# Kernel tuning notes

Hardware: AMD Instinct MI355X
Metric: run time of the kernel (lower is better)

## Reference

```python
import jax, jax.numpy as jnp
import numpy as np

B, S, E, H = 4, 2048, 1024, 16
D = E // H  # head dim = 64


def setup_inputs() -> dict:
    key = jax.random.key(0)
    ks = jax.random.split(key, 5)
    s = 0.02
    return {
        "x": jax.random.normal(ks[0], (B, S, E), dtype=jnp.float32),
        "Wq": jax.random.normal(ks[1], (E, E), dtype=jnp.float32) * s,
        "Wk": jax.random.normal(ks[2], (E, E), dtype=jnp.float32) * s,
        "Wv": jax.random.normal(ks[3], (E, E), dtype=jnp.float32) * s,
        "Wo": jax.random.normal(ks[4], (E, E), dtype=jnp.float32) * s,
        "bo": jnp.zeros((E,), dtype=jnp.float32),
    }


def reference(x, Wq, Wk, Wv, Wo, bo):
    b, s, e = x.shape
    h, d = H, e // H
    # QKV projections -> [b, h, s, d]
    q = (x @ Wq).reshape(b, s, h, d).transpose(0, 2, 1, 3)
    k = (x @ Wk).reshape(b, s, h, d).transpose(0, 2, 1, 3)
    v = (x @ Wv).reshape(b, s, h, d).transpose(0, 2, 1, 3)
    # scores [b, h, s, s], causal mask with -inf, scaled softmax
    a = jnp.einsum('bhqd,bhkd->bhqk', q, k)
    causal = jnp.tril(jnp.ones((s, s), dtype=bool))  # True where allowed
    a = jnp.where(causal, a, -jnp.inf) / jnp.sqrt(jnp.asarray(d, x.dtype))
    a = jax.nn.softmax(a, axis=-1)
    # dropout p=0.0 (identity in eval)
    y = jnp.einsum('bhqk,bhkd->bhqd', a, v)
    y = y.transpose(0, 2, 1, 3).reshape(b, s, e)
    return y @ Wo + bo
```

## Files before the change

kernel.cpp:

```cpp
#include <hip/hip_runtime.h>

typedef __bf16 bf16x8 __attribute__((ext_vector_type(8)));
typedef float f32x4 __attribute__((ext_vector_type(4)));
typedef unsigned short u16x8 __attribute__((ext_vector_type(8)));

#define S_LEN 2048
#define NHEAD 16
#define HDIM  64
#define EMB   1024

__device__ __forceinline__ ushort f2b(float v) {
  union { float f; unsigned u; } x; x.f = v;
  unsigned r = (x.u + 0x7fffu + ((x.u >> 16) & 1u)) >> 16;
  return (ushort)r;
}

__device__ __forceinline__ ushort f2b_trunc(float v) {
  union { float f; unsigned u; } x; x.f = v;
  return (ushort)(x.u >> 16);
}

typedef const __attribute__((address_space(1))) unsigned int* gp1_t;
typedef __attribute__((address_space(3))) unsigned int* lp3_t;
__device__ __forceinline__ void gld16(const ushort* g, const ushort* l) {
  __builtin_amdgcn_global_load_lds((gp1_t)(unsigned long long)(uintptr_t)g,
                                   (lp3_t)(unsigned int)(uintptr_t)l, 16, 0, 0);
}

__global__ __launch_bounds__(256) void prep_kernel(
    const float* __restrict__ x, const float* __restrict__ W0,
    const float* __restrict__ W1, const float* __restrict__ W2,
    const float* __restrict__ W3, ushort* __restrict__ xb,
    ushort* __restrict__ Wt0, ushort* __restrict__ Wt1,
    ushort* __restrict__ Wt2, ushort* __restrict__ Wt3, float scale0) {
  const int z = blockIdx.z;
  if (z == 4) {
    size_t base = ((size_t)(blockIdx.y * 32 + blockIdx.x)) * 8192 + threadIdx.x * 4;
#pragma unroll
    for (int i = 0; i < 8; ++i) {
      float4 v = *(const float4*)(x + base + i * 1024);
      ushort4 o;
      o.x = f2b(v.x); o.y = f2b(v.y); o.z = f2b(v.z); o.w = f2b(v.w);
      *(ushort4*)(xb + base + i * 1024) = o;
    }
    return;
  }
  __shared__ float t[32][33];
  const float* W = z == 0 ? W0 : (z == 1 ? W1 : (z == 2 ? W2 : W3));
  ushort* Wt = z == 0 ? Wt0 : (z == 1 ? Wt1 : (z == 2 ? Wt2 : Wt3));
  const float scale = z == 0 ? scale0 : 1.0f;
  int k0 = blockIdx.x * 32, n0 = blockIdx.y * 32;
  int c = threadIdx.x & 31, r0 = threadIdx.x >> 5;
#pragma unroll
  for (int i = 0; i < 4; ++i) {
    int r = r0 + i * 8;
    t[r][c] = W[(size_t)(k0 + r) * EMB + n0 + c];
  }
  __syncthreads();
#pragma unroll
  for (int i = 0; i < 4; ++i) {
    int r = r0 + i * 8;
    Wt[(size_t)(n0 + r) * EMB + k0 + c] = f2b(t[c][r] * scale);
  }
}

template <int EPI>
__global__ __launch_bounds__(256) void gemm_kernel(
    const ushort* __restrict__ A, const ushort* __restrict__ Bt, int K, int N,
    ushort* __restrict__ outQ, ushort* __restrict__ outK, ushort* __restrict__ outVt,
    float* __restrict__ outF, const float* __restrict__ bias) {
  __shared__ ushort As[2][128 * 32];
  __shared__ ushort Bs[2][128 * 32];
  const int tid = threadIdx.x;
  const int lane = tid & 63, ln = lane & 15, quad = lane >> 4;
  const int wave = tid >> 6, wm = wave >> 1, wn = wave & 1;
  const long m0 = (long)blockIdx.x * 128, n0 = (long)blockIdx.y * 128;

  const int sr = lane >> 2, sc = (lane & 3) * 8;
  const ushort* AgL = A + (m0 + 32 * wave + sr) * (long)K + sc;
  const ushort* BgL = Bt + (n0 + 32 * wave + sr) * (long)K + sc;

  f32x4 acc[4][4] = {};
  const int KT = K >> 5;

  {
    ushort* as = &As[0][32 * wave * 32];
    ushort* bs = &Bs[0][32 * wave * 32];
    gld16(AgL, as);
    gld16(AgL + 16 * (long)K, as + 16 * 32);
    gld16(BgL, bs);
    gld16(BgL + 16 * (long)K, bs + 16 * 32);
  }
  __syncthreads();

  for (int kt = 0; kt < KT; ++kt) {
    if (kt + 1 < KT) {
      const int nb = (kt + 1) & 1;
      const ushort* a = AgL + (kt + 1) * 32;
      const ushort* b = BgL + (kt + 1) * 32;
      ushort* as = &As[nb][32 * wave * 32];
      ushort* bs = &Bs[nb][32 * wave * 32];
      gld16(a, as);
      gld16(a + 16 * (long)K, as + 16 * 32);
      gld16(b, bs);
      gld16(b + 16 * (long)K, bs + 16 * 32);
    }
    const ushort* Ac = &As[kt & 1][0];
    const ushort* Bc = &Bs[kt & 1][0];
    bf16x8 af[4], bf[4];
#pragma unroll
    for (int mt = 0; mt < 4; ++mt)
      af[mt] = *(const bf16x8*)(Ac + (wm * 64 + mt * 16 + ln) * 32 + quad * 8);
#pragma unroll
    for (int nt = 0; nt < 4; ++nt)
      bf[nt] = *(const bf16x8*)(Bc + (wn * 64 + nt * 16 + ln) * 32 + quad * 8);
#pragma unroll
    for (int mt = 0; mt < 4; ++mt)
#pragma unroll
      for (int nt = 0; nt < 4; ++nt)
        acc[mt][nt] = __builtin_amdgcn_mfma_f32_16x16x32_bf16(af[mt], bf[nt], acc[mt][nt], 0, 0, 0);
    __syncthreads();
  }

  if (EPI == 0) {
    const int sel = (int)(n0 >> 10);
    if (sel == 2) {
#pragma unroll
      for (int mt = 0; mt < 4; ++mt) {
        const long mbase = m0 + wm * 64 + mt * 16 + quad * 4;
        const long bb = mbase >> 11, s = mbase & 2047;
#pragma unroll
        for (int nt = 0; nt < 4; ++nt) {
          const int nn = (int)((n0 & 1023) + wn * 64 + nt * 16 + ln);
          const int h = nn >> 6, d = nn & 63;
          uint2 val;
          val.x = (unsigned)f2b(acc[mt][nt][0]) | ((unsigned)f2b(acc[mt][nt][1]) << 16);
          val.y = (unsigned)f2b(acc[mt][nt][2]) | ((unsigned)f2b(acc[mt][nt][3]) << 16);
          *(uint2*)(outVt + (((bb * NHEAD + h) * (long)HDIM + d) * S_LEN) + s) = val;
        }
      }
    } else {
      ushort* dst = sel == 0 ? outQ : outK;
#pragma unroll
      for (int mt = 0; mt < 4; ++mt) {
#pragma unroll
        for (int nt = 0; nt < 4; ++nt) {
          const int nn = (int)((n0 & 1023) + wn * 64 + nt * 16 + ln);
          const int h = nn >> 6, d = nn & 63;
#pragma unroll
          for (int r = 0; r < 4; ++r) {
            const long m = m0 + wm * 64 + mt * 16 + quad * 4 + r;
            const long bb = m >> 11, s = m & 2047;
            dst[(((bb * NHEAD + h) * S_LEN) + s) * HDIM + d] = f2b(acc[mt][nt][r]);
          }
        }
      }
    }
  } else {
#pragma unroll
    for (int mt = 0; mt < 4; ++mt) {
#pragma unroll
      for (int nt = 0; nt < 4; ++nt) {
#pragma unroll
        for (int r = 0; r < 4; ++r) {
          const long m = m0 + wm * 64 + mt * 16 + quad * 4 + r;
          const long n = n0 + wn * 64 + nt * 16 + ln;
          outF[m * (long)N + n] = acc[mt][nt][r] + bias[n];
        }
      }
    }
  }
}

__global__ __launch_bounds__(256) void attn_kernel(const ushort* __restrict__ Q,
                                                   const ushort* __restrict__ Kg,
                                                   const ushort* __restrict__ Vt,
                                                   ushort* __restrict__ Y) {
  __shared__ alignas(16) ushort Ks[2][2 * 64 * 32];
  __shared__ alignas(16) ushort Vs[2][2 * 64 * 32];
  __shared__ alignas(16) ushort Ps[4 * 2 * 16 * 72];
  const int tid = threadIdx.x;
  const int wave = tid >> 6, lane = tid & 63, ln = lane & 15, quad = lane >> 4;
  const int bh = blockIdx.x;
  const int qb = 15 - (int)blockIdx.y;
  const int q0 = qb * 128;
  const size_t base = (size_t)bh * S_LEN * HDIM;
  const int ntiles = 2 * qb + 2;

  const u16x8 ob = {0x3F80, 0x3F80, 0x3F80, 0x3F80, 0x3F80, 0x3F80, 0x3F80, 0x3F80};
  const bf16x8 ones = __builtin_bit_cast(bf16x8, ob);

  bf16x8 qf[2][2];
#pragma unroll
  for (int mt = 0; mt < 2; ++mt)
#pragma unroll
    for (int ks2 = 0; ks2 < 2; ++ks2)
      qf[mt][ks2] = *(const bf16x8*)(Q + base + (size_t)(q0 + wave * 32 + mt * 16 + ln) * HDIM +
                                     ks2 * 32 + quad * 8);

  f32x4 acc[2][4] = {};
  f32x4 accl[2] = {};

  const int sr = lane >> 2, sc = (lane & 3) * 8;
  const ushort* KgL = Kg + base + (size_t)(16 * wave + sr) * HDIM + sc;
  const ushort* VgL = Vt + base + (size_t)(16 * wave + sr) * S_LEN + sc;

  {
    ushort* kb = &Ks[0][16 * wave * 32];
    ushort* vb = &Vs[0][16 * wave * 32];
    gld16(KgL, kb);
    gld16(KgL + 32, kb + 2048);
    gld16(VgL, vb);
    gld16(VgL + 32, vb + 2048);
  }
  __syncthreads();

  ushort* Pw0 = Ps + wave * 2304;
  ushort* Pw1 = Pw0 + 1152;
  const int swW = (quad >> 1) << 4;
  const int swR = (ln >> 3) << 4;

  for (int kt = 0; kt < ntiles; ++kt) {
    const int cur = kt & 1;
    const int k0 = kt * 64;
    if (kt + 1 < ntiles) {
      const int nb = cur ^ 1;
      const size_t k1 = (size_t)(k0 + 64);
      ushort* kb = &Ks[nb][16 * wave * 32];
      ushort* vb = &Vs[nb][16 * wave * 32];
      gld16(KgL + k1 * HDIM, kb);
      gld16(KgL + k1 * HDIM + 32, kb + 2048);
      gld16(VgL + k1, vb);
      gld16(VgL + k1 + 32, vb + 2048);
    }
    const ushort* Kc = &Ks[cur][0];
    const ushort* Vc = &Vs[cur][0];
    const int qbase = q0 + wave * 32;

    if (k0 < qbase + 32) {
      f32x4 s0[4] = {}, s1[4] = {};
#pragma unroll
      for (int ks2 = 0; ks2 < 2; ++ks2) {
#pragma unroll
        for (int nt = 0; nt < 4; ++nt) {
          bf16x8 bk = *(const bf16x8*)(Kc + ks2 * 2048 + (nt * 16 + ln) * 32 + quad * 8);
          s0[nt] = __builtin_amdgcn_mfma_f32_16x16x32_bf16(qf[0][ks2], bk, s0[nt], 0, 0, 0);
          s1[nt] = __builtin_amdgcn_mfma_f32_16x16x32_bf16(qf[1][ks2], bk, s1[nt], 0, 0, 0);
        }
      }

      if (k0 + 63 > qbase) {
        const int rowq = qbase + quad * 4;
#pragma unroll
        for (int nt = 0; nt < 4; ++nt)
#pragma unroll
          for (int r = 0; r < 4; ++r) {
            const int key = k0 + nt * 16 + ln;
            if (key > rowq + r) s0[nt][r] = -3.0e38f;
            if (key > rowq + 16 + r) s1[nt][r] = -3.0e38f;
          }
      }

      asm volatile("" ::: "memory");
#pragma unroll
      for (int nt = 0; nt < 4; ++nt) {
#pragma unroll
        for (int r = 0; r < 4; ++r) {
          float p0 = __builtin_amdgcn_exp2f(s0[nt][r]);
          float p1 = __builtin_amdgcn_exp2f(s1[nt][r]);
          const int row = (quad * 4 + r) * 72;
          const int col = (nt * 16 + ln) ^ swW;
          Pw0[row + col] = f2b_trunc(p0);
          Pw1[row + col] = f2b_trunc(p1);
        }
      }
      asm volatile("" ::: "memory");

#pragma unroll
      for (int ks2 = 0; ks2 < 2; ++ks2) {
        const int rcol = (ks2 * 32 + quad * 8) ^ swR;
        bf16x8 ap0 = *(const bf16x8*)(Pw0 + ln * 72 + rcol);
        bf16x8 ap1 = *(const bf16x8*)(Pw1 + ln * 72 + rcol);
        accl[0] = __builtin_amdgcn_mfma_f32_16x16x32_bf16(ap0, ones, accl[0], 0, 0, 0);
        accl[1] = __builtin_amdgcn_mfma_f32_16x16x32_bf16(ap1, ones, accl[1], 0, 0, 0);
#pragma unroll
        for (int t2 = 0; t2 < 4; ++t2) {
          bf16x8 bv = *(const bf16x8*)(Vc + ks2 * 2048 + (t2 * 16 + ln) * 32 + quad * 8);
          acc[0][t2] = __builtin_amdgcn_mfma_f32_16x16x32_bf16(ap0, bv, acc[0][t2], 0, 0, 0);
          acc[1][t2] = __builtin_amdgcn_mfma_f32_16x16x32_bf16(ap1, bv, acc[1][t2], 0, 0, 0);
        }
      }
    }
    __syncthreads();
  }

  const long b = bh >> 4;
  const int h = bh & 15;
#pragma unroll
  for (int mt = 0; mt < 2; ++mt) {
#pragma unroll
    for (int r = 0; r < 4; ++r) {
      float inv = 1.0f / accl[mt][r];
      const int qq = q0 + wave * 32 + mt * 16 + quad * 4 + r;
#pragma unroll
      for (int t2 = 0; t2 < 4; ++t2)
        Y[(((b * S_LEN + qq) * NHEAD) + h) * HDIM + t2 * 16 + ln] = f2b(acc[mt][t2][r] * inv);
    }
  }
}

extern "C" void kernel_launch(void* const* d_in, const int* in_sizes, int n_in,
                              void* d_out, int out_size, void* d_ws, size_t ws_size,
                              hipStream_t stream) {
  const float* x  = (const float*)d_in[0];
  const float* Wq = (const float*)d_in[1];
  const float* Wk = (const float*)d_in[2];
  const float* Wv = (const float*)d_in[3];
  const float* Wo = (const float*)d_in[4];
  const float* bo = (const float*)d_in[5];
  float* out = (float*)d_out;

  const size_t XE = (size_t)8192 * EMB;
  ushort* ws    = (ushort*)d_ws;
  ushort* xb    = ws;
  ushort* Wtqkv = xb + XE;
  ushort* Wto   = Wtqkv + 3 * 1048576;
  ushort* Qb    = Wto + 1048576;
  ushort* Kb    = Qb + XE;
  ushort* Vtb   = Kb + XE;
  ushort* Yb    = xb;

  const float SCALE_Q = 1.4426950408889634f / 8.0f;

  prep_kernel<<<dim3(32, 32, 5), 256, 0, stream>>>(
      x, Wq, Wk, Wv, Wo, xb, Wtqkv, Wtqkv + 1048576, Wtqkv + 2097152, Wto, SCALE_Q);

  gemm_kernel<0><<<dim3(64, 24), 256, 0, stream>>>(xb, Wtqkv, EMB, 3072,
                                                   Qb, Kb, Vtb, nullptr, nullptr);
  attn_kernel<<<dim3(64, 16), 256, 0, stream>>>(Qb, Kb, Vtb, Yb);
  gemm_kernel<1><<<dim3(64, 8), 256, 0, stream>>>(Yb, Wto, EMB, EMB,
                                                  nullptr, nullptr, nullptr, out, bo);
}
```

Measured before the change: 238.1 us.

## Switch attention kernel MFMAs from 16x16x32 to 32x32x16 tiles

Rewrites the attention inner loop to use 32x32x16 bf16 MFMA instructions instead of 16x16x32, with each wave computing a 32-row query block against 64 keys as two 32x32 tiles. The Q fragments, masking, P staging layout in LDS with its XOR swizzle, the row-sum accumulation and the output writeback are all remapped to the 32x32 accumulator layout. The aim is fewer MFMA issues and LDS fragment reads per tile. In exchange the accumulators are larger f32x16 vectors, which raises register pressure.

```diff
diff --git a/kernel.cpp b/kernel.cpp
--- a/kernel.cpp
+++ b/kernel.cpp
@@ -2,6 +2,7 @@
 
 typedef __bf16 bf16x8 __attribute__((ext_vector_type(8)));
 typedef float f32x4 __attribute__((ext_vector_type(4)));
+typedef float f32x16 __attribute__((ext_vector_type(16)));
 typedef unsigned short u16x8 __attribute__((ext_vector_type(8)));
 
 #define S_LEN 2048
@@ -178,28 +179,26 @@
                                                    ushort* __restrict__ Y) {
   __shared__ alignas(16) ushort Ks[2][2 * 64 * 32];
   __shared__ alignas(16) ushort Vs[2][2 * 64 * 32];
-  __shared__ alignas(16) ushort Ps[4 * 2 * 16 * 72];
+  __shared__ alignas(16) ushort Ps[4 * 32 * 72];
   const int tid = threadIdx.x;
-  const int wave = tid >> 6, lane = tid & 63, ln = lane & 15, quad = lane >> 4;
+  const int wave = tid >> 6, lane = tid & 63;
+  const int l5 = lane & 31, eh = lane >> 5;
   const int bh = blockIdx.x;
   const int qb = 15 - (int)blockIdx.y;
   const int q0 = qb * 128;
   const size_t base = (size_t)bh * S_LEN * HDIM;
   const int ntiles = 2 * qb + 2;
+  const int qbase = q0 + wave * 32;
 
   const u16x8 ob = {0x3F80, 0x3F80, 0x3F80, 0x3F80, 0x3F80, 0x3F80, 0x3F80, 0x3F80};
   const bf16x8 ones = __builtin_bit_cast(bf16x8, ob);
 
-  bf16x8 qf[2][2];
-#pragma unroll
-  for (int mt = 0; mt < 2; ++mt)
-#pragma unroll
-    for (int ks2 = 0; ks2 < 2; ++ks2)
-      qf[mt][ks2] = *(const bf16x8*)(Q + base + (size_t)(q0 + wave * 32 + mt * 16 + ln) * HDIM +
-                                     ks2 * 32 + quad * 8);
-
-  f32x4 acc[2][4] = {};
-  f32x4 accl[2] = {};
+  bf16x8 qf[4];
+#pragma unroll
+  for (int c = 0; c < 4; ++c)
+    qf[c] = *(const bf16x8*)(Q + base + (size_t)(qbase + l5) * HDIM + c * 16 + eh * 8);
+
+  f32x16 acc0 = {}, acc1 = {}, accl = {};
 
   const int sr = lane >> 2, sc = (lane & 3) * 8;
   const ushort* KgL = Kg + base + (size_t)(16 * wave + sr) * HDIM + sc;
@@ -215,10 +214,7 @@
   }
   __syncthreads();
 
-  ushort* Pw0 = Ps + wave * 2304;
-  ushort* Pw1 = Pw0 + 1152;
-  const int swW = (quad >> 1) << 4;
-  const int swR = (ln >> 3) << 4;
+  ushort* Pw = Ps + wave * 32 * 72;
 
   for (int kt = 0; kt < ntiles; ++kt) {
     const int cur = kt & 1;
@@ -235,60 +231,54 @@
     }
     const ushort* Kc = &Ks[cur][0];
     const ushort* Vc = &Vs[cur][0];
-    const int qbase = q0 + wave * 32;
-
-    if (k0 < qbase + 32) {
-      f32x4 s0[4] = {}, s1[4] = {};
-#pragma unroll
-      for (int ks2 = 0; ks2 < 2; ++ks2) {
-#pragma unroll
-        for (int nt = 0; nt < 4; ++nt) {
-          bf16x8 bk = *(const bf16x8*)(Kc + ks2 * 2048 + (nt * 16 + ln) * 32 + quad * 8);
-          s0[nt] = __builtin_amdgcn_mfma_f32_16x16x32_bf16(qf[0][ks2], bk, s0[nt], 0, 0, 0);
-          s1[nt] = __builtin_amdgcn_mfma_f32_16x16x32_bf16(qf[1][ks2], bk, s1[nt], 0, 0, 0);
+
+    if (k0 <= qbase + 31) {
+      f32x16 s0 = {}, s1 = {};
+#pragma unroll
+      for (int c = 0; c < 4; ++c) {
+        const int doff = (c >> 1) * 2048 + (c & 1) * 16 + eh * 8;
+        bf16x8 bk0 = *(const bf16x8*)(Kc + doff + l5 * 32);
+        bf16x8 bk1 = *(const bf16x8*)(Kc + doff + (32 + l5) * 32);
+        s0 = __builtin_amdgcn_mfma_f32_32x32x16_bf16(qf[c], bk0, s0, 0, 0, 0);
+        s1 = __builtin_amdgcn_mfma_f32_32x32x16_bf16(qf[c], bk1, s1, 0, 0, 0);
+      }
+
+      if (k0 + 63 > qbase) {
+#pragma unroll
+        for (int g = 0; g < 4; ++g)
+#pragma unroll
+          for (int r = 0; r < 4; ++r) {
+            const int row = qbase + r + 8 * g + 4 * eh;
+            if (k0 + l5 > row) s0[4 * g + r] = -3.0e38f;
+            if (k0 + 32 + l5 > row) s1[4 * g + r] = -3.0e38f;
+          }
+      }
+
+      asm volatile("" ::: "memory");
+#pragma unroll
+      for (int g = 0; g < 4; ++g) {
+        const int sw = (g & 1) << 4;
+#pragma unroll
+        for (int r = 0; r < 4; ++r) {
+          const int rowoff = (r + 8 * g + 4 * eh) * 72;
+          float p0 = __builtin_amdgcn_exp2f(s0[4 * g + r]);
+          float p1 = __builtin_amdgcn_exp2f(s1[4 * g + r]);
+          Pw[rowoff + (l5 ^ sw)] = f2b_trunc(p0);
+          Pw[rowoff + ((32 + l5) ^ sw)] = f2b_trunc(p1);
         }
       }
-
-      if (k0 + 63 > qbase) {
-        const int rowq = qbase + quad * 4;
-#pragma unroll
-        for (int nt = 0; nt < 4; ++nt)
-#pragma unroll
-          for (int r = 0; r < 4; ++r) {
-            const int key = k0 + nt * 16 + ln;
-            if (key > rowq + r) s0[nt][r] = -3.0e38f;
-            if (key > rowq + 16 + r) s1[nt][r] = -3.0e38f;
-          }
-      }
-
       asm volatile("" ::: "memory");
-#pragma unroll
-      for (int nt = 0; nt < 4; ++nt) {
-#pragma unroll
-        for (int r = 0; r < 4; ++r) {
-          float p0 = __builtin_amdgcn_exp2f(s0[nt][r]);
-          float p1 = __builtin_amdgcn_exp2f(s1[nt][r]);
-          const int row = (quad * 4 + r) * 72;
-          const int col = (nt * 16 + ln) ^ swW;
-          Pw0[row + col] = f2b_trunc(p0);
-          Pw1[row + col] = f2b_trunc(p1);
-        }
-      }
-      asm volatile("" ::: "memory");
-
-#pragma unroll
-      for (int ks2 = 0; ks2 < 2; ++ks2) {
-        const int rcol = (ks2 * 32 + quad * 8) ^ swR;
-        bf16x8 ap0 = *(const bf16x8*)(Pw0 + ln * 72 + rcol);
-        bf16x8 ap1 = *(const bf16x8*)(Pw1 + ln * 72 + rcol);
-        accl[0] = __builtin_amdgcn_mfma_f32_16x16x32_bf16(ap0, ones, accl[0], 0, 0, 0);
-        accl[1] = __builtin_amdgcn_mfma_f32_16x16x32_bf16(ap1, ones, accl[1], 0, 0, 0);
-#pragma unroll
-        for (int t2 = 0; t2 < 4; ++t2) {
-          bf16x8 bv = *(const bf16x8*)(Vc + ks2 * 2048 + (t2 * 16 + ln) * 32 + quad * 8);
-          acc[0][t2] = __builtin_amdgcn_mfma_f32_16x16x32_bf16(ap0, bv, acc[0][t2], 0, 0, 0);
-          acc[1][t2] = __builtin_amdgcn_mfma_f32_16x16x32_bf16(ap1, bv, acc[1][t2], 0, 0, 0);
-        }
+
+      const int rsw = ((l5 >> 3) & 1) << 4;
+#pragma unroll
+      for (int c = 0; c < 4; ++c) {
+        bf16x8 ap = *(const bf16x8*)(Pw + l5 * 72 + ((c * 16 + eh * 8) ^ rsw));
+        const int koff = (c >> 1) * 2048 + (c & 1) * 16 + eh * 8;
+        bf16x8 bv0 = *(const bf16x8*)(Vc + koff + l5 * 32);
+        bf16x8 bv1 = *(const bf16x8*)(Vc + koff + (32 + l5) * 32);
+        acc0 = __builtin_amdgcn_mfma_f32_32x32x16_bf16(ap, bv0, acc0, 0, 0, 0);
+        acc1 = __builtin_amdgcn_mfma_f32_32x32x16_bf16(ap, bv1, acc1, 0, 0, 0);
+        accl = __builtin_amdgcn_mfma_f32_32x32x16_bf16(ap, ones, accl, 0, 0, 0);
       }
     }
     __syncthreads();
@@ -297,14 +287,15 @@
   const long b = bh >> 4;
   const int h = bh & 15;
 #pragma unroll
-  for (int mt = 0; mt < 2; ++mt) {
+  for (int g = 0; g < 4; ++g) {
 #pragma unroll
     for (int r = 0; r < 4; ++r) {
-      float inv = 1.0f / accl[mt][r];
-      const int qq = q0 + wave * 32 + mt * 16 + quad * 4 + r;
-#pragma unroll
-      for (int t2 = 0; t2 < 4; ++t2)
-        Y[(((b * S_LEN + qq) * NHEAD) + h) * HDIM + t2 * 16 + ln] = f2b(acc[mt][t2][r] * inv);
+      const int ri = 4 * g + r;
+      float inv = 1.0f / accl[ri];
+      const int qq = qbase + r + 8 * g + 4 * eh;
+      ushort* yr = Y + (((b * S_LEN + qq) * NHEAD) + h) * HDIM;
+      yr[l5] = f2b(acc0[ri] * inv);
+      yr[32 + l5] = f2b(acc1[ri] * inv);
     }
   }
 }
```

Measured after the change: 262.7 us. 1.1x slower.
